# Kernel tuning notes

Measured on AMD Instinct MI355X. Metric: run time of the kernel, lower is better.

The kernel has to match this reference:

```python
import jax, jax.numpy as jnp
import numpy as np

COMMITMENT_COST = 0.25
DECAY = 0.99
EPSILON = 1e-05


def setup_inputs() -> dict:
    key = jax.random.key(0)
    k1, k2, k3, k4 = jax.random.split(key, 4)
    S, B, D, K = 256, 64, 512, 4096
    return {
        "inputs": jax.random.normal(k1, (S, B, D), dtype=jnp.float32),
        "embedding_weight": jax.random.normal(k2, (K, D), dtype=jnp.float32),
        "ema_w": jax.random.normal(k3, (K, D), dtype=jnp.float32),
        "ema_cluster_size": jax.random.uniform(k4, (K,), dtype=jnp.float32),
    }


def reference(inputs, embedding_weight, ema_w, ema_cluster_size):
    S, B, D = inputs.shape
    K = embedding_weight.shape[0]
    flat = inputs.reshape(-1, D)  # [N, D], N = S*B

    distances = (
        jnp.sum(flat * flat, axis=1, keepdims=True)
        + jnp.sum(embedding_weight * embedding_weight, axis=1)
        - 2.0 * flat @ embedding_weight.T
    )
    encoding_indices = jnp.argmin(distances, axis=1)  # [N]
    encodings = jax.nn.one_hot(encoding_indices, K, dtype=inputs.dtype)  # [N, K]

    # gather codebook rows (equivalent to encodings @ weight)
    quantized = jnp.take(embedding_weight, encoding_indices, axis=0).reshape(S, B, D)
    encodings_flat = encodings.reshape(S, B, K)

    # EMA codebook update (training-mode buffers; computed with stop_gradient semantics)
    counts = jnp.sum(encodings, axis=0)  # [K]
    new_cluster_size = ema_cluster_size * DECAY + (1.0 - DECAY) * counts
    n = jnp.sum(new_cluster_size)
    new_cluster_size = (new_cluster_size + EPSILON) / (n + K * EPSILON) * n
    dw = jax.ops.segment_sum(flat, encoding_indices, num_segments=K)  # encodings.T @ flat
    new_ema_w = ema_w * DECAY + (1.0 - DECAY) * dw
    new_embedding_weight = new_ema_w / new_cluster_size[:, None]

    # commitment loss (quantized detached)
    e_latent_loss = jnp.mean((jax.lax.stop_gradient(quantized) - inputs) ** 2)
    loss = COMMITMENT_COST * e_latent_loss

    # straight-through estimator
    quantized_st = inputs + jax.lax.stop_gradient(quantized - inputs)

    return (
        loss,
        quantized_st,
        encodings_flat,
        encoding_indices[:, None],
        new_embedding_weight,
        new_cluster_size,
        new_ema_w,
    )
```

## Files before the change

### kernel.cpp

```cpp
#include <hip/hip_runtime.h>
#include <hip/hip_bf16.h>
#include <cstdint>
#include <cstddef>

typedef __attribute__((ext_vector_type(8))) short short8;
typedef __attribute__((ext_vector_type(4))) float f32x4;

#define D_DIM 512
#define K_DIM 4096
#define N_ROWS 16384

#define DECAY_F 0.99f
#define OMD_F 0.01f
#define EPS_F 1e-5f
#define COMMIT_F 0.25f
#define MARGIN_F 0.75f

#define OFF_LOSS 0
#define OFF_QST 1
#define OFF_ENC (1 + 8388608)
#define OFF_IDX (OFF_ENC + 67108864)
#define OFF_NEW_W (OFF_IDX + 16384)
#define OFF_NEW_CS (OFF_NEW_W + 2097152)
#define OFF_NEW_EMA (OFF_NEW_CS + 4096)

#define WS_MINKEY 0
#define WS_COUNTS 131072
#define WS_E2 147456
#define WS_LOSSP 163840
#define WS_RCNT 164096
#define WS_OFFS 164112
#define WS_CURS 180496
#define WS_ROWL 196880
#define WS_ARENA 262416

#define AR_M1K 0
#define AR_M2V 4194304
#define AR_XHI 6291456
#define AR_EHI 23068672
#define AR_RROW 27262976
#define AR_RCUT 27328512
#define AR_NEED 27394048
#define WS_NEED (WS_ARENA + AR_NEED)

#define SCR0 8388612

__device__ __forceinline__ unsigned long long mkkey(float d, int c) {
  unsigned u = __float_as_uint(d);
  u ^= (unsigned)(((int)u) >> 31) | 0x80000000u;
  return ((unsigned long long)u << 32) | (unsigned)c;
}
__device__ __forceinline__ float keyval(unsigned long long k) {
  unsigned u = (unsigned)(k >> 32);
  u = (u & 0x80000000u) ? (u ^ 0x80000000u) : ~u;
  return __uint_as_float(u);
}
__device__ __forceinline__ void merge2(unsigned long long& k1, float& v2,
                                       unsigned long long ko, float v2o) {
  float v1 = keyval(k1), v1o = keyval(ko);
  float vmax = fmaxf(v1, v1o);
  v2 = fminf(fminf(v2, v2o), vmax);
  if (ko < k1) k1 = ko;
}
__device__ __forceinline__ unsigned pk2o(float a, float b) {
  unsigned ua = (__float_as_uint(a) + 0x8000u) & 0xFFFF0000u;
  unsigned ub = (__float_as_uint(b) + 0x8000u) & 0xFFFF0000u;
  return (ua >> 16) | ub;
}
__device__ __forceinline__ void gl_lds16(const void* g, void* l) {
  __builtin_amdgcn_global_load_lds(
      (const __attribute__((address_space(1))) unsigned int*)g,
      (__attribute__((address_space(3))) unsigned int*)l, 16, 0, 0);
}

__global__ void k_e2(const float* __restrict__ E, float* __restrict__ e2,
                     uint4* __restrict__ ehi, int* __restrict__ counts,
                     float* __restrict__ loss_part, int* __restrict__ rcnt) {
  int tid = threadIdx.x;
  int lane = tid & 63;
  int w = tid >> 6;
  int k = blockIdx.x * 4 + w;
  if (tid < 4) counts[blockIdx.x * 4 + tid] = 0;
  if (blockIdx.x == 0 && tid < 64) loss_part[tid] = 0.f;
  if (blockIdx.x == 1 && tid == 0) *rcnt = 0;
  const float4* ev = (const float4*)(E + (size_t)k * D_DIM);
  float4 a = ev[lane * 2], b = ev[lane * 2 + 1];
  uint4 h;
  h.x = pk2o(a.x, a.y);
  h.y = pk2o(a.z, a.w);
  h.z = pk2o(b.x, b.y);
  h.w = pk2o(b.z, b.w);
  ehi[(size_t)k * 64 + lane] = h;
  float s = a.x * a.x + a.y * a.y + a.z * a.z + a.w * a.w +
            b.x * b.x + b.y * b.y + b.z * b.z + b.w * b.w;
#pragma unroll
  for (int off = 32; off > 0; off >>= 1) s += __shfl_down(s, off, 64);
  if (lane == 0) e2[k] = s;
}

__global__ void k_conv(const float* __restrict__ src, uint4* __restrict__ hi) {
  int t = blockIdx.x * 256 + threadIdx.x;
  const float4* s4 = (const float4*)src;
  float4 a = s4[t * 2], b = s4[t * 2 + 1];
  uint4 h;
  h.x = pk2o(a.x, a.y);
  h.y = pk2o(a.z, a.w);
  h.z = pk2o(b.x, b.y);
  h.w = pk2o(b.z, b.w);
  hi[t] = h;
}

__global__ void k_scale_emaw(const float* __restrict__ ema_w, float* __restrict__ out) {
  int i = blockIdx.x * 256 + threadIdx.x;
  out[OFF_NEW_EMA + i] = DECAY_F * ema_w[i];
}

__global__ __launch_bounds__(256, 2) void k_gemm(
    const char* __restrict__ xhi, const char* __restrict__ ehi,
    const float* __restrict__ e2, unsigned long long* __restrict__ m1k,
    float* __restrict__ m2v, float* outp, int doZero) {
  extern __shared__ char smem[];
  const int tid = threadIdx.x;
  const int w = tid >> 6, lane = tid & 63;
  const int wr = w >> 1, wc = w & 1;
  const int l15 = lane & 15, g = lane >> 4;
  const int row0 = blockIdx.x * 128;
  const int col0 = blockIdx.y * 128;

  const char* srcBase = (w < 2) ? xhi : ehi;
  const int srcRow0 = (w < 2) ? (row0 + 64 * w) : (col0 + 64 * (w - 2));
  const int lr = lane >> 3;
  const int lc = lane & 7;
  const char* srcLane = srcBase + (size_t)(srcRow0 + lr) * 1024 + ((lc ^ lr) << 4);
  const int dstOff = w * 8192;

#define STAGE(c, b)                                       \
  {                                                       \
    const char* sp_ = srcLane + (c) * 128;                \
    char* lb_ = smem + (b) * 32768 + dstOff;              \
    _Pragma("unroll") for (int q = 0; q < 8; ++q)         \
        gl_lds16(sp_ + q * 8192, lb_ + q * 1024);         \
  }

  f32x4 acc[4][4];
  const f32x4 z = {0.f, 0.f, 0.f, 0.f};
#pragma unroll
  for (int i = 0; i < 4; ++i)
#pragma unroll
    for (int j = 0; j < 4; ++j) acc[i][j] = z;

  STAGE(0, 0);
  const int s0 = (g ^ (l15 & 7)) << 4;
  const int aRow = (wr * 64 + l15) * 128;
  const int bRow = (wc * 64 + l15) * 128;

  for (int c = 0; c < 8; ++c) {
    __syncthreads();
    if (c < 7) STAGE(c + 1, (c + 1) & 1);
    const char* Ab = smem + (c & 1) * 32768;
    const char* Bb = Ab + 16384;
    short8 a[2][4], b[2][4];
#pragma unroll
    for (int kk = 0; kk < 2; ++kk) {
      const int sw = s0 ^ (kk << 6);
#pragma unroll
      for (int i = 0; i < 4; ++i) {
        a[kk][i] = *(const short8*)(Ab + aRow + i * 2048 + sw);
        b[kk][i] = *(const short8*)(Bb + bRow + i * 2048 + sw);
      }
    }
#pragma unroll
    for (int kk = 0; kk < 2; ++kk)
#pragma unroll
      for (int i = 0; i < 4; ++i)
#pragma unroll
        for (int j = 0; j < 4; ++j)
          acc[i][j] = __builtin_amdgcn_mfma_f32_16x16x32_bf16(a[kk][i], b[kk][j], acc[i][j], 0, 0, 0);
  }
#undef STAGE

  __syncthreads();
  unsigned long long* lk = (unsigned long long*)smem;
  float* lv = (float*)(smem + 2048);
  float e2v[4];
#pragma unroll
  for (int j = 0; j < 4; ++j) e2v[j] = e2[col0 + wc * 64 + j * 16 + l15];

#pragma unroll
  for (int i = 0; i < 4; ++i) {
    int rowl = wr * 64 + i * 16 + (g << 2);
#pragma unroll
    for (int r = 0; r < 4; ++r) {
      unsigned long long k1 = 0;
      float v2 = 3.4e38f;
#pragma unroll
      for (int j = 0; j < 4; ++j) {
        float dv = fmaf(-2.f, acc[i][j][r], e2v[j]);
        unsigned long long kk = mkkey(dv, col0 + wc * 64 + j * 16 + l15);
        if (j == 0) k1 = kk;
        else merge2(k1, v2, kk, 3.4e38f);
      }
#pragma unroll
      for (int m = 1; m <= 8; m <<= 1) {
        unsigned long long ko = __shfl_xor(k1, m, 64);
        float vo = __shfl_xor(v2, m, 64);
        merge2(k1, v2, ko, vo);
      }
      if (l15 == 0) {
        lk[(rowl + r) * 2 + wc] = k1;
        lv[(rowl + r) * 2 + wc] = v2;
      }
    }
  }
  __syncthreads();
  if (tid < 128) {
    unsigned long long k1 = lk[tid * 2];
    float v2 = lv[tid * 2];
    merge2(k1, v2, lk[tid * 2 + 1], lv[tid * 2 + 1]);
    size_t o = (size_t)(row0 + tid) * 32 + blockIdx.y;
    m1k[o] = k1;
    m2v[o] = v2;
  }

  if (doZero) {
    const f32x4 z4 = {0.f, 0.f, 0.f, 0.f};
    float* encm1 = outp + (size_t)OFF_ENC - 1 + (size_t)row0 * K_DIM + col0;
#pragma unroll
    for (int q = 0; q < 16; ++q) {
      int s = tid + 256 * q;
      int r = s >> 5, c4 = s & 31;
      float* p = encm1 + (size_t)r * K_DIM + c4 * 4;
      if (row0 == 0 && col0 == 0 && s == 0) {
        outp[OFF_ENC + 0] = 0.f;
        outp[OFF_ENC + 1] = 0.f;
        outp[OFF_ENC + 2] = 0.f;
      } else {
        __builtin_nontemporal_store(z4, (f32x4*)p);
      }
    }
  }
}

__global__ void k_reduce(const unsigned long long* __restrict__ m1k,
                         const float* __restrict__ m2v,
                         unsigned long long* __restrict__ minkey,
                         int* __restrict__ rcnt, int* __restrict__ rrows,
                         float* __restrict__ rcut) {
  int row = blockIdx.x * 256 + threadIdx.x;
  const unsigned long long* kp = m1k + (size_t)row * 32;
  const float* vp = m2v + (size_t)row * 32;
  unsigned long long k1 = kp[0];
  float v2 = vp[0];
#pragma unroll 4
  for (int t = 1; t < 32; ++t) merge2(k1, v2, kp[t], vp[t]);
  float v1 = keyval(k1);
  if (v2 - v1 < MARGIN_F) {
    minkey[row] = ~0ull;
    int p = atomicAdd(rcnt, 1);
    rrows[p] = row;
    rcut[p] = v1 + MARGIN_F;
  } else {
    minkey[row] = k1;
  }
}

__global__ __launch_bounds__(256) void k_rescue(
    const float* __restrict__ flat, const float* __restrict__ E,
    const float* __restrict__ e2, const int* __restrict__ rcnt,
    const int* __restrict__ rrows, const float* __restrict__ rcut,
    const unsigned long long* __restrict__ m1k,
    unsigned long long* __restrict__ minkey) {
  __shared__ float sx[512];
  __shared__ unsigned long long skey[16];
  const int tid = threadIdx.x;
  const int sl = tid & 15;
  int cnt = *rcnt;
  if (cnt > N_ROWS) cnt = N_ROWS;
  for (int j = (int)blockIdx.x; j < cnt; j += (int)gridDim.x) {
    const int row = rrows[j];
    const float cutoff = rcut[j];
    __syncthreads();
    if (tid < 128) ((float4*)sx)[tid] = ((const float4*)(flat + (size_t)row * 512))[tid];
    __syncthreads();
    unsigned long long best = ~0ull;
    for (int b = 0; b < 32; ++b) {
      if (keyval(m1k[(size_t)row * 32 + b]) >= cutoff) continue;
      const int c0 = b * 128 + (tid >> 4);
#pragma unroll 2
      for (int p = 0; p < 8; ++p) {
        const int c = c0 + p * 16;
        const float4* ev = (const float4*)(E + (size_t)c * 512) + sl * 8;
        const float4* xv = (const float4*)sx + sl * 8;
        float s = 0.f;
#pragma unroll
        for (int q = 0; q < 8; ++q) {
          float4 e4 = ev[q];
          float4 x4 = xv[q];
          s = fmaf(e4.x, x4.x, s);
          s = fmaf(e4.y, x4.y, s);
          s = fmaf(e4.z, x4.z, s);
          s = fmaf(e4.w, x4.w, s);
        }
#pragma unroll
        for (int m = 1; m <= 8; m <<= 1) s += __shfl_xor(s, m, 64);
        if (sl == 0) {
          unsigned long long k = mkkey(fmaf(-2.f, s, e2[c]), c);
          if (k < best) best = k;
        }
      }
    }
    if (sl == 0) skey[tid >> 4] = best;
    __syncthreads();
    if (tid == 0) {
      unsigned long long m = skey[0];
#pragma unroll
      for (int t = 1; t < 16; ++t)
        if (skey[t] < m) m = skey[t];
      atomicMin(&minkey[row], m);
    }
  }
}

__global__ void k_zero(float* __restrict__ out) {
  const f32x4 z = {0.f, 0.f, 0.f, 0.f};
  f32x4* out4 = (f32x4*)(out + 8388612);
#pragma unroll
  for (int t = 0; t < 4; ++t) {
    int i = blockIdx.x * 1024 + t * 256 + threadIdx.x;
    if (i < 16777215) __builtin_nontemporal_store(z, out4 + i);
  }
  if (blockIdx.x == 0 && threadIdx.x == 0) {
    out[8388609] = 0.f;
    out[8388610] = 0.f;
    out[8388611] = 0.f;
    out[75497472] = 0.f;
  }
}

__global__ void k_decode(const unsigned long long* __restrict__ minkey,
                         int* __restrict__ counts, float* __restrict__ out) {
  int n = blockIdx.x * 256 + threadIdx.x;
  int c = (int)(unsigned)(minkey[n] & 0xffffffffull);
  out[OFF_IDX + n] = (float)c;
  atomicAdd(&counts[c], 1);
  if (n == N_ROWS - 1) out[(size_t)OFF_ENC + (size_t)n * K_DIM + 4095] = 0.f;
  out[(size_t)OFF_ENC + (size_t)n * K_DIM + c] = 1.0f;
}

__global__ __launch_bounds__(1024) void k_prefix(const int* __restrict__ counts,
                                                 int* __restrict__ offs,
                                                 int* __restrict__ cursor) {
  __shared__ int wsum[16];
  const int tid = threadIdx.x;
  const int lane = tid & 63, w = tid >> 6;
  int v[4];
  int loc = 0;
#pragma unroll
  for (int t = 0; t < 4; ++t) {
    v[t] = counts[tid * 4 + t];
    loc += v[t];
  }
  int scan = loc;
#pragma unroll
  for (int off = 1; off <= 32; off <<= 1) {
    int o = __shfl_up(scan, off, 64);
    if (lane >= off) scan += o;
  }
  if (lane == 63) wsum[w] = scan;
  __syncthreads();
  int base = 0;
  for (int i = 0; i < w; ++i) base += wsum[i];
  int run = base + scan - loc;
#pragma unroll
  for (int t = 0; t < 4; ++t) {
    offs[tid * 4 + t] = run;
    cursor[tid * 4 + t] = run;
    run += v[t];
  }
}

__global__ void k_scatter(const unsigned long long* __restrict__ minkey,
                          int* __restrict__ cursor, int* __restrict__ rowl) {
  int n = blockIdx.x * 256 + threadIdx.x;
  int c = (int)(unsigned)(minkey[n] & 0xffffffffull);
  int pos = atomicAdd(&cursor[c], 1);
  rowl[pos] = n;
}

__global__ __launch_bounds__(256) void k_dw(const float* __restrict__ flat,
                                            const float* __restrict__ ema_w,
                                            const int* __restrict__ counts,
                                            const int* __restrict__ offs,
                                            const int* __restrict__ rowl,
                                            float* __restrict__ out) {
  const int k = blockIdx.x;
  const int tid = threadIdx.x;
  const int cnt = counts[k];
  const int off = offs[k];
  const int d0 = tid * 2;
  float s0 = 0.f, s1 = 0.f;
  for (int i = 0; i < cnt; ++i) {
    int r = rowl[off + i];
    float2 x = *(const float2*)(flat + (size_t)r * D_DIM + d0);
    s0 += x.x;
    s1 += x.y;
  }
  float e0 = DECAY_F * ema_w[(size_t)k * D_DIM + d0] + OMD_F * s0;
  float e1 = DECAY_F * ema_w[(size_t)k * D_DIM + d0 + 1] + OMD_F * s1;
  float cs = out[OFF_NEW_CS + k];
  size_t b = (size_t)k * D_DIM + d0;
  out[OFF_NEW_EMA + b] = e0;
  out[OFF_NEW_EMA + b + 1] = e1;
  out[OFF_NEW_W + b] = e0 / cs;
  out[OFF_NEW_W + b + 1] = e1 / cs;
}

__global__ void k_quant(const float* __restrict__ flat, const float* __restrict__ E,
                        const unsigned long long* __restrict__ minkey,
                        float* __restrict__ out, float* emaw,
                        float* __restrict__ loss_part) {
  int tid = threadIdx.x;
  int lane = tid & 63;
  int rw = tid >> 6;
  int n = blockIdx.x * 4 + rw;
  int idx = (int)(unsigned)(minkey[n] & 0xffffffffull);
  const float4* xv = (const float4*)(flat + (size_t)n * D_DIM);
  const float4* ev = (const float4*)(E + (size_t)idx * D_DIM);
  float* emarow = emaw ? emaw + (size_t)idx * D_DIM : nullptr;
  float s = 0.f;
#pragma unroll
  for (int t = 0; t < 2; ++t) {
    int p = lane + 64 * t;
    float4 x = xv[p];
    float4 e = ev[p];
    size_t qb = (size_t)OFF_QST + (size_t)n * D_DIM + (size_t)p * 4;
    out[qb + 0] = x.x + (e.x - x.x);
    out[qb + 1] = x.y + (e.y - x.y);
    out[qb + 2] = x.z + (e.z - x.z);
    out[qb + 3] = x.w + (e.w - x.w);
    float dx = e.x - x.x, dy = e.y - x.y, dz = e.z - x.z, dw = e.w - x.w;
    s += dx * dx + dy * dy + dz * dz + dw * dw;
    if (emarow) {
      atomicAdd(emarow + p * 4 + 0, OMD_F * x.x);
      atomicAdd(emarow + p * 4 + 1, OMD_F * x.y);
      atomicAdd(emarow + p * 4 + 2, OMD_F * x.z);
      atomicAdd(emarow + p * 4 + 3, OMD_F * x.w);
    }
  }
#pragma unroll
  for (int off = 32; off > 0; off >>= 1) s += __shfl_down(s, off, 64);
  __shared__ float ws4[4];
  if (lane == 0) ws4[rw] = s;
  __syncthreads();
  if (tid == 0) atomicAdd(&loss_part[blockIdx.x & 63], ws4[0] + ws4[1] + ws4[2] + ws4[3]);
}

__global__ __launch_bounds__(1024) void k_cs(const float* __restrict__ ema_cs,
                                             const int* __restrict__ counts,
                                             const float* __restrict__ loss_part,
                                             float* __restrict__ out) {
  int tid = threadIdx.x;
  float cs1[4];
  float local = 0.f;
#pragma unroll
  for (int t = 0; t < 4; ++t) {
    int k = tid + 1024 * t;
    cs1[t] = ema_cs[k] * DECAY_F + OMD_F * (float)counts[k];
    local += cs1[t];
  }
  __shared__ float wsum[16];
  float v = local;
#pragma unroll
  for (int off = 32; off > 0; off >>= 1) v += __shfl_down(v, off, 64);
  if ((tid & 63) == 0) wsum[tid >> 6] = v;
  __syncthreads();
  float n_total = 0.f;
#pragma unroll
  for (int t = 0; t < 16; ++t) n_total += wsum[t];
  float scale = n_total / (n_total + (float)K_DIM * EPS_F);
#pragma unroll
  for (int t = 0; t < 4; ++t) {
    int k = tid + 1024 * t;
    out[OFF_NEW_CS + k] = (cs1[t] + EPS_F) * scale;
  }
  if (tid < 64) {
    float lv = loss_part[tid];
#pragma unroll
    for (int off = 32; off > 0; off >>= 1) lv += __shfl_down(lv, off, 64);
    if (tid == 0) out[OFF_LOSS] = COMMIT_F * lv / 8388608.0f;
  }
}

__global__ void k_final(float* __restrict__ out) {
  int i = blockIdx.x * 256 + threadIdx.x;
  int k = i >> 9;
  out[OFF_NEW_W + i] = out[OFF_NEW_EMA + i] / out[OFF_NEW_CS + k];
}

extern "C" void kernel_launch(void* const* d_in, const int* in_sizes, int n_in,
                              void* d_out, int out_size, void* d_ws, size_t ws_size,
                              hipStream_t stream) {
  (void)in_sizes; (void)n_in; (void)out_size;
  const float* flat = (const float*)d_in[0];
  const float* E = (const float*)d_in[1];
  const float* ema_w = (const float*)d_in[2];
  const float* ema_cs = (const float*)d_in[3];
  float* out = (float*)d_out;
  char* ws = (char*)d_ws;

  unsigned long long* minkey = (unsigned long long*)(ws + WS_MINKEY);
  int* counts = (int*)(ws + WS_COUNTS);
  float* e2 = (float*)(ws + WS_E2);
  float* loss_part = (float*)(ws + WS_LOSSP);
  int* rcnt = (int*)(ws + WS_RCNT);
  int* offs = (int*)(ws + WS_OFFS);
  int* cursor = (int*)(ws + WS_CURS);
  int* rowl = (int*)(ws + WS_ROWL);

  const bool big = ws_size >= (size_t)WS_NEED;
  char* arena = big ? (ws + WS_ARENA) : (char*)(out + SCR0);
  unsigned long long* m1k = (unsigned long long*)(arena + AR_M1K);
  float* m2v = (float*)(arena + AR_M2V);
  char* xhi = arena + AR_XHI;
  char* ehi = arena + AR_EHI;
  int* rrows = (int*)(arena + AR_RROW);
  float* rcut = (float*)(arena + AR_RCUT);

  k_e2<<<1024, 256, 0, stream>>>(E, e2, (uint4*)ehi, counts, loss_part, rcnt);
  k_conv<<<4096, 256, 0, stream>>>(flat, (uint4*)xhi);
  if (!big) k_scale_emaw<<<8192, 256, 0, stream>>>(ema_w, out);
  k_gemm<<<dim3(128, 32), 256, 65536, stream>>>(xhi, ehi, e2, m1k, m2v, out, big ? 1 : 0);
  k_reduce<<<64, 256, 0, stream>>>(m1k, m2v, minkey, rcnt, rrows, rcut);
  k_rescue<<<2048, 256, 0, stream>>>(flat, E, e2, rcnt, rrows, rcut, m1k, minkey);
  if (big) {
    k_decode<<<64, 256, 0, stream>>>(minkey, counts, out);
    k_prefix<<<1, 1024, 0, stream>>>(counts, offs, cursor);
    k_scatter<<<64, 256, 0, stream>>>(minkey, cursor, rowl);
    k_quant<<<4096, 256, 0, stream>>>(flat, E, minkey, out, nullptr, loss_part);
    k_cs<<<1, 1024, 0, stream>>>(ema_cs, counts, loss_part, out);
    k_dw<<<4096, 256, 0, stream>>>(flat, ema_w, counts, offs, rowl, out);
  } else {
    k_zero<<<16384, 256, 0, stream>>>(out);
    k_decode<<<64, 256, 0, stream>>>(minkey, counts, out);
    k_quant<<<4096, 256, 0, stream>>>(flat, E, minkey, out, out + OFF_NEW_EMA, loss_part);
    k_cs<<<1, 1024, 0, stream>>>(ema_cs, counts, loss_part, out);
    k_final<<<8192, 256, 0, stream>>>(out);
  }
}
```

Baseline: 412.4 us.

## Spread encoding-buffer cleanup across kernels as extra blocks with read-before-write

Removes the bulk zeroing of the one-hot encodings tile from the GEMM epilogue. The cleanup is split into 2048 chunks handed out as extra blocks appended to the GEMM, rescue, quant and dw launches, so it overlaps with compute-bound work. Each chunk reads the buffer and only writes zeros where a value is nonzero, which cuts write traffic when the buffer is already mostly zero, at the cost of a full read pass. Per-code counts move into an LDS histogram inside k_prefix, and the one-hot decode runs last without atomics.

```diff
diff --git a/kernel.cpp b/kernel.cpp
--- a/kernel.cpp
+++ b/kernel.cpp
@@ -5,6 +5,7 @@
 
 typedef __attribute__((ext_vector_type(8))) short short8;
 typedef __attribute__((ext_vector_type(4))) float f32x4;
+typedef __attribute__((ext_vector_type(4))) unsigned int u32x4;
 
 #define D_DIM 512
 #define K_DIM 4096
@@ -23,6 +24,10 @@
 #define OFF_NEW_W (OFF_IDX + 16384)
 #define OFF_NEW_CS (OFF_NEW_W + 2097152)
 #define OFF_NEW_EMA (OFF_NEW_CS + 4096)
+
+#define ENC4_BASE 8388612
+#define ENC4_CNT 16777215
+#define CHUNK4 8192
 
 #define WS_MINKEY 0
 #define WS_COUNTS 131072
@@ -71,6 +76,27 @@
   __builtin_amdgcn_global_load_lds(
       (const __attribute__((address_space(1))) unsigned int*)g,
       (__attribute__((address_space(3))) unsigned int*)l, 16, 0, 0);
+}
+
+__device__ __forceinline__ void clean_chunk(float* __restrict__ out, int cid) {
+  const int tid = threadIdx.x;
+  const f32x4 z = {0.f, 0.f, 0.f, 0.f};
+  const u32x4* p = (const u32x4*)(out + ENC4_BASE);
+  const int base = cid * CHUNK4;
+#pragma unroll
+  for (int t = 0; t < 32; ++t) {
+    int i = base + t * 256 + tid;
+    if (i < ENC4_CNT) {
+      u32x4 v = __builtin_nontemporal_load(p + i);
+      if (v.x | v.y | v.z | v.w) *(f32x4*)(p + i) = z;
+    }
+  }
+  if (cid == 0 && tid == 0) {
+    if (__float_as_uint(out[8388609])) out[8388609] = 0.f;
+    if (__float_as_uint(out[8388610])) out[8388610] = 0.f;
+    if (__float_as_uint(out[8388611])) out[8388611] = 0.f;
+    if (__float_as_uint(out[75497472])) out[75497472] = 0.f;
+  }
 }
 
 __global__ void k_e2(const float* __restrict__ E, float* __restrict__ e2,
@@ -118,7 +144,11 @@
 __global__ __launch_bounds__(256, 2) void k_gemm(
     const char* __restrict__ xhi, const char* __restrict__ ehi,
     const float* __restrict__ e2, unsigned long long* __restrict__ m1k,
-    float* __restrict__ m2v, float* outp, int doZero) {
+    float* __restrict__ m2v, float* outp) {
+  if (blockIdx.x >= 128) {
+    clean_chunk(outp, (blockIdx.x - 128) * 32 + blockIdx.y);
+    return;
+  }
   extern __shared__ char smem[];
   const int tid = threadIdx.x;
   const int w = tid >> 6, lane = tid & 63;
@@ -220,24 +250,6 @@
     size_t o = (size_t)(row0 + tid) * 32 + blockIdx.y;
     m1k[o] = k1;
     m2v[o] = v2;
-  }
-
-  if (doZero) {
-    const f32x4 z4 = {0.f, 0.f, 0.f, 0.f};
-    float* encm1 = outp + (size_t)OFF_ENC - 1 + (size_t)row0 * K_DIM + col0;
-#pragma unroll
-    for (int q = 0; q < 16; ++q) {
-      int s = tid + 256 * q;
-      int r = s >> 5, c4 = s & 31;
-      float* p = encm1 + (size_t)r * K_DIM + c4 * 4;
-      if (row0 == 0 && col0 == 0 && s == 0) {
-        outp[OFF_ENC + 0] = 0.f;
-        outp[OFF_ENC + 1] = 0.f;
-        outp[OFF_ENC + 2] = 0.f;
-      } else {
-        __builtin_nontemporal_store(z4, (f32x4*)p);
-      }
-    }
   }
 }
 
@@ -269,14 +281,18 @@
     const float* __restrict__ e2, const int* __restrict__ rcnt,
     const int* __restrict__ rrows, const float* __restrict__ rcut,
     const unsigned long long* __restrict__ m1k,
-    unsigned long long* __restrict__ minkey) {
+    unsigned long long* __restrict__ minkey, float* outp, int nmain, int cbase) {
+  if ((int)blockIdx.x >= nmain) {
+    clean_chunk(outp, cbase + (int)blockIdx.x - nmain);
+    return;
+  }
   __shared__ float sx[512];
   __shared__ unsigned long long skey[16];
   const int tid = threadIdx.x;
   const int sl = tid & 15;
   int cnt = *rcnt;
   if (cnt > N_ROWS) cnt = N_ROWS;
-  for (int j = (int)blockIdx.x; j < cnt; j += (int)gridDim.x) {
+  for (int j = (int)blockIdx.x; j < cnt; j += nmain) {
     const int row = rrows[j];
     const float cutoff = rcut[j];
     __syncthreads();
@@ -337,27 +353,28 @@
   }
 }
 
-__global__ void k_decode(const unsigned long long* __restrict__ minkey,
-                         int* __restrict__ counts, float* __restrict__ out) {
-  int n = blockIdx.x * 256 + threadIdx.x;
-  int c = (int)(unsigned)(minkey[n] & 0xffffffffull);
-  out[OFF_IDX + n] = (float)c;
-  atomicAdd(&counts[c], 1);
-  if (n == N_ROWS - 1) out[(size_t)OFF_ENC + (size_t)n * K_DIM + 4095] = 0.f;
-  out[(size_t)OFF_ENC + (size_t)n * K_DIM + c] = 1.0f;
-}
-
-__global__ __launch_bounds__(1024) void k_prefix(const int* __restrict__ counts,
+__global__ __launch_bounds__(1024) void k_prefix(const unsigned long long* __restrict__ minkey,
+                                                 int* __restrict__ counts,
                                                  int* __restrict__ offs,
                                                  int* __restrict__ cursor) {
+  __shared__ int lc[4096];
   __shared__ int wsum[16];
   const int tid = threadIdx.x;
   const int lane = tid & 63, w = tid >> 6;
+#pragma unroll
+  for (int t = 0; t < 4; ++t) lc[tid * 4 + t] = 0;
+  __syncthreads();
+#pragma unroll
+  for (int t = 0; t < 16; ++t) {
+    int c = (int)(unsigned)(minkey[tid + 1024 * t] & 0xffffffffull);
+    atomicAdd(&lc[c], 1);
+  }
+  __syncthreads();
   int v[4];
   int loc = 0;
 #pragma unroll
   for (int t = 0; t < 4; ++t) {
-    v[t] = counts[tid * 4 + t];
+    v[t] = lc[tid * 4 + t];
     loc += v[t];
   }
   int scan = loc;
@@ -373,6 +390,7 @@
   int run = base + scan - loc;
 #pragma unroll
   for (int t = 0; t < 4; ++t) {
+    counts[tid * 4 + t] = v[t];
     offs[tid * 4 + t] = run;
     cursor[tid * 4 + t] = run;
     run += v[t];
@@ -392,7 +410,11 @@
                                             const int* __restrict__ counts,
                                             const int* __restrict__ offs,
                                             const int* __restrict__ rowl,
-                                            float* __restrict__ out) {
+                                            float* __restrict__ out, int cbase) {
+  if (blockIdx.x >= K_DIM) {
+    clean_chunk(out, cbase + (int)blockIdx.x - K_DIM);
+    return;
+  }
   const int k = blockIdx.x;
   const int tid = threadIdx.x;
   const int cnt = counts[k];
@@ -418,7 +440,11 @@
 __global__ void k_quant(const float* __restrict__ flat, const float* __restrict__ E,
                         const unsigned long long* __restrict__ minkey,
                         float* __restrict__ out, float* emaw,
-                        float* __restrict__ loss_part) {
+                        float* __restrict__ loss_part, int cbase) {
+  if (blockIdx.x >= 4096) {
+    clean_chunk(out, cbase + (int)blockIdx.x - 4096);
+    return;
+  }
   int tid = threadIdx.x;
   int lane = tid & 63;
   int rw = tid >> 6;
@@ -455,6 +481,16 @@
   if (tid == 0) atomicAdd(&loss_part[blockIdx.x & 63], ws4[0] + ws4[1] + ws4[2] + ws4[3]);
 }
 
+__global__ void k_decode(const unsigned long long* __restrict__ minkey,
+                         int* __restrict__ counts, float* __restrict__ out,
+                         int withCounts) {
+  int n = blockIdx.x * 256 + threadIdx.x;
+  int c = (int)(unsigned)(minkey[n] & 0xffffffffull);
+  out[OFF_IDX + n] = (float)c;
+  if (withCounts) atomicAdd(&counts[c], 1);
+  out[(size_t)OFF_ENC + (size_t)n * K_DIM + c] = 1.0f;
+}
+
 __global__ __launch_bounds__(1024) void k_cs(const float* __restrict__ ema_cs,
                                              const int* __restrict__ counts,
                                              const float* __restrict__ loss_part,
@@ -528,21 +564,27 @@
 
   k_e2<<<1024, 256, 0, stream>>>(E, e2, (uint4*)ehi, counts, loss_part, rcnt);
   k_conv<<<4096, 256, 0, stream>>>(flat, (uint4*)xhi);
-  if (!big) k_scale_emaw<<<8192, 256, 0, stream>>>(ema_w, out);
-  k_gemm<<<dim3(128, 32), 256, 65536, stream>>>(xhi, ehi, e2, m1k, m2v, out, big ? 1 : 0);
-  k_reduce<<<64, 256, 0, stream>>>(m1k, m2v, minkey, rcnt, rrows, rcut);
-  k_rescue<<<2048, 256, 0, stream>>>(flat, E, e2, rcnt, rrows, rcut, m1k, minkey);
   if (big) {
-    k_decode<<<64, 256, 0, stream>>>(minkey, counts, out);
-    k_prefix<<<1, 1024, 0, stream>>>(counts, offs, cursor);
+    k_gemm<<<dim3(164, 32), 256, 65536, stream>>>(xhi, ehi, e2, m1k, m2v, out);
+    k_reduce<<<64, 256, 0, stream>>>(m1k, m2v, minkey, rcnt, rrows, rcut);
+    k_rescue<<<2304, 256, 0, stream>>>(flat, E, e2, rcnt, rrows, rcut, m1k, minkey,
+                                       out, 2048, 1152);
+    k_prefix<<<1, 1024, 0, stream>>>(minkey, counts, offs, cursor);
     k_scatter<<<64, 256, 0, stream>>>(minkey, cursor, rowl);
-    k_quant<<<4096, 256, 0, stream>>>(flat, E, minkey, out, nullptr, loss_part);
+    k_quant<<<4416, 256, 0, stream>>>(flat, E, minkey, out, nullptr, loss_part, 1408);
     k_cs<<<1, 1024, 0, stream>>>(ema_cs, counts, loss_part, out);
-    k_dw<<<4096, 256, 0, stream>>>(flat, ema_w, counts, offs, rowl, out);
+    k_dw<<<4416, 256, 0, stream>>>(flat, ema_w, counts, offs, rowl, out, 1728);
+    k_decode<<<64, 256, 0, stream>>>(minkey, counts, out, 0);
   } else {
+    k_scale_emaw<<<8192, 256, 0, stream>>>(ema_w, out);
+    k_gemm<<<dim3(128, 32), 256, 65536, stream>>>(xhi, ehi, e2, m1k, m2v, out);
+    k_reduce<<<64, 256, 0, stream>>>(m1k, m2v, minkey, rcnt, rrows, rcut);
+    k_rescue<<<2048, 256, 0, stream>>>(flat, E, e2, rcnt, rrows, rcut, m1k, minkey,
+                                       out, 2048, 0);
     k_zero<<<16384, 256, 0, stream>>>(out);
-    k_decode<<<64, 256, 0, stream>>>(minkey, counts, out);
-    k_quant<<<4096, 256, 0, stream>>>(flat, E, minkey, out, out + OFF_NEW_EMA, loss_part);
+    k_decode<<<64, 256, 0, stream>>>(minkey, counts, out, 1);
+    k_quant<<<4096, 256, 0, stream>>>(flat, E, minkey, out, out + OFF_NEW_EMA,
+                                      loss_part, 0);
     k_cs<<<1, 1024, 0, stream>>>(ema_cs, counts, loss_part, out);
     k_final<<<8192, 256, 0, stream>>>(out);
   }
```

After: 469.4 us. +13.8%, slower.

## Fuse quantize and loss into per-code dw kernel, count codes in shared memory

Applied to the files above, without the earlier changes.

On the large-workspace path, the quantized straight-through output and commitment loss are now computed inside the per-codebook-row dw kernel, which already walks each code's assigned rows. This removes the separate k_quant pass that re-read the inputs and gathered E rows. Code counts are built with shared-memory atomics inside the single-block prefix kernel instead of global atomics in k_decode. k_decode now runs last and also finalizes the loss. The fused kernel uses scalar 2-float loads with scattered row writes per block and has load imbalance across popular codes, and the histogram is serialized into one block.

```diff
diff --git a/kernel.cpp b/kernel.cpp
--- a/kernel.cpp
+++ b/kernel.cpp
@@ -337,27 +337,28 @@
   }
 }
 
-__global__ void k_decode(const unsigned long long* __restrict__ minkey,
-                         int* __restrict__ counts, float* __restrict__ out) {
-  int n = blockIdx.x * 256 + threadIdx.x;
-  int c = (int)(unsigned)(minkey[n] & 0xffffffffull);
-  out[OFF_IDX + n] = (float)c;
-  atomicAdd(&counts[c], 1);
-  if (n == N_ROWS - 1) out[(size_t)OFF_ENC + (size_t)n * K_DIM + 4095] = 0.f;
-  out[(size_t)OFF_ENC + (size_t)n * K_DIM + c] = 1.0f;
-}
-
-__global__ __launch_bounds__(1024) void k_prefix(const int* __restrict__ counts,
+__global__ __launch_bounds__(1024) void k_prefix(const unsigned long long* __restrict__ minkey,
+                                                 int* __restrict__ counts,
                                                  int* __restrict__ offs,
                                                  int* __restrict__ cursor) {
+  __shared__ int lc[4096];
   __shared__ int wsum[16];
   const int tid = threadIdx.x;
   const int lane = tid & 63, w = tid >> 6;
+#pragma unroll
+  for (int t = 0; t < 4; ++t) lc[tid * 4 + t] = 0;
+  __syncthreads();
+#pragma unroll
+  for (int t = 0; t < 16; ++t) {
+    int c = (int)(unsigned)(minkey[tid + 1024 * t] & 0xffffffffull);
+    atomicAdd(&lc[c], 1);
+  }
+  __syncthreads();
   int v[4];
   int loc = 0;
 #pragma unroll
   for (int t = 0; t < 4; ++t) {
-    v[t] = counts[tid * 4 + t];
+    v[t] = lc[tid * 4 + t];
     loc += v[t];
   }
   int scan = loc;
@@ -373,6 +374,7 @@
   int run = base + scan - loc;
 #pragma unroll
   for (int t = 0; t < 4; ++t) {
+    counts[tid * 4 + t] = v[t];
     offs[tid * 4 + t] = run;
     cursor[tid * 4 + t] = run;
     run += v[t];
@@ -387,23 +389,33 @@
   rowl[pos] = n;
 }
 
-__global__ __launch_bounds__(256) void k_dw(const float* __restrict__ flat,
-                                            const float* __restrict__ ema_w,
-                                            const int* __restrict__ counts,
-                                            const int* __restrict__ offs,
-                                            const int* __restrict__ rowl,
-                                            float* __restrict__ out) {
+__global__ __launch_bounds__(256) void k_qdw(const float* __restrict__ flat,
+                                             const float* __restrict__ E,
+                                             const float* __restrict__ ema_w,
+                                             const int* __restrict__ counts,
+                                             const int* __restrict__ offs,
+                                             const int* __restrict__ rowl,
+                                             float* __restrict__ out,
+                                             float* __restrict__ loss_part) {
   const int k = blockIdx.x;
   const int tid = threadIdx.x;
   const int cnt = counts[k];
   const int off = offs[k];
   const int d0 = tid * 2;
-  float s0 = 0.f, s1 = 0.f;
+  const float ex = E[(size_t)k * D_DIM + d0];
+  const float ey = E[(size_t)k * D_DIM + d0 + 1];
+  float s0 = 0.f, s1 = 0.f, lsum = 0.f;
   for (int i = 0; i < cnt; ++i) {
     int r = rowl[off + i];
-    float2 x = *(const float2*)(flat + (size_t)r * D_DIM + d0);
-    s0 += x.x;
-    s1 += x.y;
+    const float* xr = flat + (size_t)r * D_DIM + d0;
+    float xx = xr[0], xy = xr[1];
+    size_t qb = (size_t)OFF_QST + (size_t)r * D_DIM + d0;
+    out[qb] = xx + (ex - xx);
+    out[qb + 1] = xy + (ey - xy);
+    float dx = ex - xx, dy = ey - xy;
+    lsum += dx * dx + dy * dy;
+    s0 += xx;
+    s1 += xy;
   }
   float e0 = DECAY_F * ema_w[(size_t)k * D_DIM + d0] + OMD_F * s0;
   float e1 = DECAY_F * ema_w[(size_t)k * D_DIM + d0 + 1] + OMD_F * s1;
@@ -413,6 +425,13 @@
   out[OFF_NEW_EMA + b + 1] = e1;
   out[OFF_NEW_W + b] = e0 / cs;
   out[OFF_NEW_W + b + 1] = e1 / cs;
+#pragma unroll
+  for (int o = 32; o > 0; o >>= 1) lsum += __shfl_down(lsum, o, 64);
+  __shared__ float ws4[4];
+  if ((tid & 63) == 0) ws4[tid >> 6] = lsum;
+  __syncthreads();
+  if (tid == 0 && cnt > 0)
+    atomicAdd(&loss_part[k & 63], ws4[0] + ws4[1] + ws4[2] + ws4[3]);
 }
 
 __global__ void k_quant(const float* __restrict__ flat, const float* __restrict__ E,
@@ -426,7 +445,7 @@
   int idx = (int)(unsigned)(minkey[n] & 0xffffffffull);
   const float4* xv = (const float4*)(flat + (size_t)n * D_DIM);
   const float4* ev = (const float4*)(E + (size_t)idx * D_DIM);
-  float* emarow = emaw ? emaw + (size_t)idx * D_DIM : nullptr;
+  float* emarow = emaw + (size_t)idx * D_DIM;
   float s = 0.f;
 #pragma unroll
   for (int t = 0; t < 2; ++t) {
@@ -440,12 +459,10 @@
     out[qb + 3] = x.w + (e.w - x.w);
     float dx = e.x - x.x, dy = e.y - x.y, dz = e.z - x.z, dw = e.w - x.w;
     s += dx * dx + dy * dy + dz * dz + dw * dw;
-    if (emarow) {
-      atomicAdd(emarow + p * 4 + 0, OMD_F * x.x);
-      atomicAdd(emarow + p * 4 + 1, OMD_F * x.y);
-      atomicAdd(emarow + p * 4 + 2, OMD_F * x.z);
-      atomicAdd(emarow + p * 4 + 3, OMD_F * x.w);
-    }
+    atomicAdd(emarow + p * 4 + 0, OMD_F * x.x);
+    atomicAdd(emarow + p * 4 + 1, OMD_F * x.y);
+    atomicAdd(emarow + p * 4 + 2, OMD_F * x.z);
+    atomicAdd(emarow + p * 4 + 3, OMD_F * x.w);
   }
 #pragma unroll
   for (int off = 32; off > 0; off >>= 1) s += __shfl_down(s, off, 64);
@@ -455,10 +472,28 @@
   if (tid == 0) atomicAdd(&loss_part[blockIdx.x & 63], ws4[0] + ws4[1] + ws4[2] + ws4[3]);
 }
 
+__global__ void k_decode(const unsigned long long* __restrict__ minkey,
+                         int* __restrict__ counts,
+                         const float* __restrict__ loss_part,
+                         float* __restrict__ out, int withCounts, int withLoss) {
+  int n = blockIdx.x * 256 + threadIdx.x;
+  int c = (int)(unsigned)(minkey[n] & 0xffffffffull);
+  out[OFF_IDX + n] = (float)c;
+  if (withCounts) atomicAdd(&counts[c], 1);
+  if (n == N_ROWS - 1) out[(size_t)OFF_ENC + (size_t)n * K_DIM + 4095] = 0.f;
+  out[(size_t)OFF_ENC + (size_t)n * K_DIM + c] = 1.0f;
+  if (withLoss && blockIdx.x == 0 && threadIdx.x < 64) {
+    float lv = loss_part[threadIdx.x];
+#pragma unroll
+    for (int off = 32; off > 0; off >>= 1) lv += __shfl_down(lv, off, 64);
+    if (threadIdx.x == 0) out[OFF_LOSS] = COMMIT_F * lv / 8388608.0f;
+  }
+}
+
 __global__ __launch_bounds__(1024) void k_cs(const float* __restrict__ ema_cs,
                                              const int* __restrict__ counts,
                                              const float* __restrict__ loss_part,
-                                             float* __restrict__ out) {
+                                             float* __restrict__ out, int withLoss) {
   int tid = threadIdx.x;
   float cs1[4];
   float local = 0.f;
@@ -483,7 +518,7 @@
     int k = tid + 1024 * t;
     out[OFF_NEW_CS + k] = (cs1[t] + EPS_F) * scale;
   }
-  if (tid < 64) {
+  if (withLoss && tid < 64) {
     float lv = loss_part[tid];
 #pragma unroll
     for (int off = 32; off > 0; off >>= 1) lv += __shfl_down(lv, off, 64);
@@ -528,22 +563,24 @@
 
   k_e2<<<1024, 256, 0, stream>>>(E, e2, (uint4*)ehi, counts, loss_part, rcnt);
   k_conv<<<4096, 256, 0, stream>>>(flat, (uint4*)xhi);
-  if (!big) k_scale_emaw<<<8192, 256, 0, stream>>>(ema_w, out);
-  k_gemm<<<dim3(128, 32), 256, 65536, stream>>>(xhi, ehi, e2, m1k, m2v, out, big ? 1 : 0);
-  k_reduce<<<64, 256, 0, stream>>>(m1k, m2v, minkey, rcnt, rrows, rcut);
-  k_rescue<<<2048, 256, 0, stream>>>(flat, E, e2, rcnt, rrows, rcut, m1k, minkey);
   if (big) {
-    k_decode<<<64, 256, 0, stream>>>(minkey, counts, out);
-    k_prefix<<<1, 1024, 0, stream>>>(counts, offs, cursor);
+    k_gemm<<<dim3(128, 32), 256, 65536, stream>>>(xhi, ehi, e2, m1k, m2v, out, 1);
+    k_reduce<<<64, 256, 0, stream>>>(m1k, m2v, minkey, rcnt, rrows, rcut);
+    k_rescue<<<2048, 256, 0, stream>>>(flat, E, e2, rcnt, rrows, rcut, m1k, minkey);
+    k_prefix<<<1, 1024, 0, stream>>>(minkey, counts, offs, cursor);
     k_scatter<<<64, 256, 0, stream>>>(minkey, cursor, rowl);
-    k_quant<<<4096, 256, 0, stream>>>(flat, E, minkey, out, nullptr, loss_part);
-    k_cs<<<1, 1024, 0, stream>>>(ema_cs, counts, loss_part, out);
-    k_dw<<<4096, 256, 0, stream>>>(flat, ema_w, counts, offs, rowl, out);
+    k_cs<<<1, 1024, 0, stream>>>(ema_cs, counts, loss_part, out, 0);
+    k_qdw<<<4096, 256, 0, stream>>>(flat, E, ema_w, counts, offs, rowl, out, loss_part);
+    k_decode<<<64, 256, 0, stream>>>(minkey, counts, loss_part, out, 0, 1);
   } else {
+    k_scale_emaw<<<8192, 256, 0, stream>>>(ema_w, out);
+    k_gemm<<<dim3(128, 32), 256, 65536, stream>>>(xhi, ehi, e2, m1k, m2v, out, 0);
+    k_reduce<<<64, 256, 0, stream>>>(m1k, m2v, minkey, rcnt, rrows, rcut);
+    k_rescue<<<2048, 256, 0, stream>>>(flat, E, e2, rcnt, rrows, rcut, m1k, minkey);
     k_zero<<<16384, 256, 0, stream>>>(out);
-    k_decode<<<64, 256, 0, stream>>>(minkey, counts, out);
+    k_decode<<<64, 256, 0, stream>>>(minkey, counts, loss_part, out, 1, 0);
     k_quant<<<4096, 256, 0, stream>>>(flat, E, minkey, out, out + OFF_NEW_EMA, loss_part);
-    k_cs<<<1, 1024, 0, stream>>>(ema_cs, counts, loss_part, out);
+    k_cs<<<1, 1024, 0, stream>>>(ema_cs, counts, loss_part, out, 1);
     k_final<<<8192, 256, 0, stream>>>(out);
   }
 }
```

After: 391.2 us. 1.05x faster.
